# Kernel tuning notes

Measured on AMD Instinct MI355X. Metric: run time of the kernel, lower is better.

The kernel has to match this reference:

```python
import jax, jax.numpy as jnp
import numpy as np

B, N, IN_DIM, HID = 8, 4096, 256, 256


def setup_inputs() -> dict:
    key = jax.random.key(0)
    ks = jax.random.split(key, 7)
    s_in = 1.0 / np.sqrt(IN_DIM)
    return {
        "x": jax.random.normal(ks[0], (B, N, IN_DIM), dtype=jnp.float32),
        "Wq": jax.random.uniform(ks[1], (IN_DIM, HID), jnp.float32, -s_in, s_in),
        "bq": jax.random.uniform(ks[2], (HID,), jnp.float32, -s_in, s_in),
        "Wk": jax.random.uniform(ks[3], (IN_DIM, HID), jnp.float32, -s_in, s_in),
        "bk": jax.random.uniform(ks[4], (HID,), jnp.float32, -s_in, s_in),
        "Wv": jax.random.uniform(ks[5], (IN_DIM, HID), jnp.float32, -s_in, s_in),
        "bv": jax.random.uniform(ks[6], (HID,), jnp.float32, -s_in, s_in),
    }


def reference(x, Wq, bq, Wk, bk, Wv, bv):
    # x: [B, N, in_dim]
    Q = jnp.einsum("bnd,dh->bnh", x, Wq) + bq  # [B, N, H]
    K = jnp.einsum("bnd,dh->bnh", x, Wk) + bk
    V = jnp.einsum("bnd,dh->bnh", x, Wv) + bv
    scale = 1.0 / jnp.sqrt(jnp.asarray(K.shape[-1], dtype=x.dtype))
    scores = jnp.einsum("bqh,bkh->bqk", Q, K) * scale  # [B, N, N]
    attn = jax.nn.softmax(scores, axis=-1)
    out = jnp.einsum("bqk,bkh->bqh", attn, V)  # [B, N, H]
    return out.mean(axis=1)  # [B, H]
```

## Files before the change

### kernel.cpp

```cpp
#include <hip/hip_runtime.h>
#include <hip/hip_bf16.h>


#define NTOK 4096
#define HDIM 256
#define NBATCH 8
#define SCALE 0.0625f

typedef __attribute__((ext_vector_type(8))) short short8_t;
typedef __attribute__((ext_vector_type(16))) float f32x16;

__device__ __forceinline__ unsigned short f2bf(float f) {
    unsigned u = __float_as_uint(f);
    u += 0x7fff + ((u >> 16) & 1);
    return (unsigned short)(u >> 16);
}

#define MFMA(a, b, c) __builtin_amdgcn_mfma_f32_32x32x16_bf16(a, b, c, 0, 0, 0)

__device__ __forceinline__ void async_cp16(const void* g, void* l) {
    __builtin_amdgcn_global_load_lds((const __attribute__((address_space(1))) void*)g,
                                     (__attribute__((address_space(3))) void*)l, 16, 0, 0);
}

__device__ __forceinline__ void stage_swz(unsigned short* lds, const unsigned short* src,
                                          int row0, int dbase, int w, int l) {
#pragma unroll
    for (int i = 0; i < 4; ++i) {
        int rloc = w * 32 + i * 8 + (l >> 3);
        int u = (l & 7) ^ (l >> 3);
        const unsigned short* g = src + (size_t)(row0 + rloc) * HDIM + dbase + u * 8;
        unsigned short* d = lds + (w * 32 + i * 8) * 64;
        async_cp16(g, d);
    }
}

__device__ __forceinline__ short8_t frd(const unsigned short* lds, int rb, int lo, int u) {
    return *(const short8_t*)(lds + ((rb * 32 + lo) * 8 + (u ^ (lo & 7))) * 8);
}

__global__ void zero_kernel(float* __restrict__ w, float* __restrict__ l, float* __restrict__ out) {
    int i = blockIdx.x * 256 + threadIdx.x;
    w[i] = 0.f;
    l[i] = 0.f;
    if (i < NBATCH * HDIM) out[i] = 0.f;
}

__global__ void convert_x(const float* __restrict__ x, unsigned short* __restrict__ xbf) {
    int i = (blockIdx.x * 256 + threadIdx.x) * 4;
    float4 v = *(const float4*)(x + i);
    ushort4 o;
    o.x = f2bf(v.x); o.y = f2bf(v.y); o.z = f2bf(v.z); o.w = f2bf(v.w);
    *(ushort4*)(xbf + i) = o;
}

__global__ void convert_wt(const float* __restrict__ Wq, const float* __restrict__ Wk,
                           const float* __restrict__ Wv, unsigned short* __restrict__ Wt) {
    int z = blockIdx.y;
    const float* W = (z == 0) ? Wq : (z == 1) ? Wk : Wv;
    unsigned short* o = Wt + z * 65536;
    int n = threadIdx.x;
    for (int kk = 0; kk < 32; ++kk) {
        int k = blockIdx.x * 32 + kk;
        o[n * 256 + k] = f2bf(W[k * 256 + n]);
    }
}

__global__ __launch_bounds__(256) void qkv_mfma(const unsigned short* __restrict__ xbf,
                                                const unsigned short* __restrict__ Wt,
                                                const float* __restrict__ bq, const float* __restrict__ bk,
                                                const float* __restrict__ bv,
                                                unsigned short* __restrict__ Qbf,
                                                unsigned short* __restrict__ Kbf,
                                                float* __restrict__ Vf) {
    const int z = blockIdx.z;
    const unsigned short* Wz = Wt + z * 65536;
    const float* bias = (z == 0) ? bq : (z == 1) ? bk : bv;
    const int m0 = blockIdx.x * 128, n0 = blockIdx.y * 128;
    const int t = threadIdx.x, w = t >> 6, l = t & 63, lo = l & 31, hi = l >> 5;
    const int rm = (w & 1) * 2, rn = (w >> 1) * 2;

    __shared__ __align__(16) char smem[32768];
    unsigned short* Xb = (unsigned short*)smem;
    unsigned short* Wb = (unsigned short*)(smem + 16384);

    f32x16 acc[2][2];
#pragma unroll
    for (int a = 0; a < 2; ++a)
#pragma unroll
        for (int c = 0; c < 2; ++c)
#pragma unroll
            for (int r = 0; r < 16; ++r) acc[a][c][r] = 0.f;

    for (int dc = 0; dc < 4; ++dc) {
        __syncthreads();
        stage_swz(Xb, xbf, m0, dc * 64, w, l);
        stage_swz(Wb, Wz, n0, dc * 64, w, l);
        __syncthreads();
#pragma unroll
        for (int ks = 0; ks < 4; ++ks) {
            int u = ks * 2 + hi;
            short8_t a0 = frd(Xb, rm + 0, lo, u);
            short8_t a1 = frd(Xb, rm + 1, lo, u);
            short8_t b0 = frd(Wb, rn + 0, lo, u);
            short8_t b1 = frd(Wb, rn + 1, lo, u);
            acc[0][0] = MFMA(a0, b0, acc[0][0]);
            acc[0][1] = MFMA(a0, b1, acc[0][1]);
            acc[1][0] = MFMA(a1, b0, acc[1][0]);
            acc[1][1] = MFMA(a1, b1, acc[1][1]);
        }
    }
    float bc0 = bias[n0 + (w >> 1) * 64 + lo];
    float bc1 = bias[n0 + (w >> 1) * 64 + 32 + lo];
#pragma unroll
    for (int mb = 0; mb < 2; ++mb)
#pragma unroll
        for (int r = 0; r < 16; ++r) {
            int row = m0 + (w & 1) * 64 + mb * 32 + (r & 3) + 8 * (r >> 2) + 4 * hi;
            int c0 = n0 + (w >> 1) * 64 + lo, c1 = c0 + 32;
            float v0 = acc[mb][0][r] + bc0;
            float v1 = acc[mb][1][r] + bc1;
            if (z == 2) {
                Vf[(size_t)row * HDIM + c0] = v0;
                Vf[(size_t)row * HDIM + c1] = v1;
            } else {
                unsigned short* o = (z == 0) ? Qbf : Kbf;
                o[(size_t)row * HDIM + c0] = f2bf(v0);
                o[(size_t)row * HDIM + c1] = f2bf(v1);
            }
        }
}

__global__ __launch_bounds__(256) void score_pass1(const unsigned short* __restrict__ Qbf,
                                                   const unsigned short* __restrict__ Kbf,
                                                   float* __restrict__ lsum) {
    const int b = blockIdx.z;
    const int q0 = blockIdx.x * 128;
    const int kslice = blockIdx.y;
    const int t = threadIdx.x, w = t >> 6, l = t & 63, lo = l & 31, hi = l >> 5;
    const int rq = (w & 1) * 2, rk = (w >> 1) * 2;
    const unsigned short* Qb = Qbf + (size_t)b * NTOK * HDIM;
    const unsigned short* Kb = Kbf + (size_t)b * NTOK * HDIM;

    __shared__ __align__(16) char smem[33792];
    unsigned short* Qs = (unsigned short*)smem;
    unsigned short* Ks = Qs + 8192;
    float* red = (float*)smem;

    float rs[2][16];
#pragma unroll
    for (int mb = 0; mb < 2; ++mb)
#pragma unroll
        for (int r = 0; r < 16; ++r) rs[mb][r] = 0.f;

    for (int kt = 0; kt < 4; ++kt) {
        const int k0 = kslice * 512 + kt * 128;
        f32x16 acc[2][2];
#pragma unroll
        for (int a = 0; a < 2; ++a)
#pragma unroll
            for (int c = 0; c < 2; ++c)
#pragma unroll
                for (int r = 0; r < 16; ++r) acc[a][c][r] = 0.f;

        for (int dc = 0; dc < 4; ++dc) {
            __syncthreads();
            stage_swz(Qs, Qb, q0, dc * 64, w, l);
            stage_swz(Ks, Kb, k0, dc * 64, w, l);
            __syncthreads();
#pragma unroll
            for (int ks = 0; ks < 4; ++ks) {
                int u = ks * 2 + hi;
                short8_t a0 = frd(Qs, rq + 0, lo, u);
                short8_t a1 = frd(Qs, rq + 1, lo, u);
                short8_t b0 = frd(Ks, rk + 0, lo, u);
                short8_t b1 = frd(Ks, rk + 1, lo, u);
                acc[0][0] = MFMA(a0, b0, acc[0][0]);
                acc[0][1] = MFMA(a0, b1, acc[0][1]);
                acc[1][0] = MFMA(a1, b0, acc[1][0]);
                acc[1][1] = MFMA(a1, b1, acc[1][1]);
            }
        }
#pragma unroll
        for (int mb = 0; mb < 2; ++mb)
#pragma unroll
            for (int r = 0; r < 16; ++r)
                rs[mb][r] += __expf(acc[mb][0][r] * SCALE) + __expf(acc[mb][1][r] * SCALE);
    }
    __syncthreads();
#pragma unroll
    for (int mb = 0; mb < 2; ++mb)
#pragma unroll
        for (int r = 0; r < 16; ++r) {
            int row = (w & 1) * 64 + mb * 32 + (r & 3) + 8 * (r >> 2) + 4 * hi;
            red[row * 66 + (w >> 1) * 32 + lo] = rs[mb][r];
        }
    __syncthreads();
    if (t < 128) {
        float s = 0.f;
#pragma unroll 8
        for (int j = 0; j < 64; ++j) s += red[t * 66 + j];
        atomicAdd(&lsum[b * NTOK + q0 + t], s);
    }
}

__global__ __launch_bounds__(256) void score_pass2(const unsigned short* __restrict__ Qbf,
                                                   const unsigned short* __restrict__ Kbf,
                                                   const float* __restrict__ lsum,
                                                   float* __restrict__ wsum) {
    const int b = blockIdx.z;
    const int k0 = blockIdx.x * 128;
    const int qslice = blockIdx.y;
    const int t = threadIdx.x, w = t >> 6, l = t & 63, lo = l & 31, hi = l >> 5;
    const int rq = (w & 1) * 2, rk = (w >> 1) * 2;
    const unsigned short* Qb = Qbf + (size_t)b * NTOK * HDIM;
    const unsigned short* Kb = Kbf + (size_t)b * NTOK * HDIM;

    __shared__ __align__(16) char smem[33792];
    __shared__ float linv_s[128];
    unsigned short* Qs = (unsigned short*)smem;
    unsigned short* Ks = Qs + 8192;
    float* red2 = (float*)smem;

    float cs0 = 0.f, cs1 = 0.f;

    for (int qt = 0; qt < 4; ++qt) {
        const int q0 = qslice * 512 + qt * 128;
        f32x16 acc[2][2];
#pragma unroll
        for (int a = 0; a < 2; ++a)
#pragma unroll
            for (int c = 0; c < 2; ++c)
#pragma unroll
                for (int r = 0; r < 16; ++r) acc[a][c][r] = 0.f;

        for (int dc = 0; dc < 4; ++dc) {
            __syncthreads();
            stage_swz(Qs, Qb, q0, dc * 64, w, l);
            stage_swz(Ks, Kb, k0, dc * 64, w, l);
            if (dc == 0 && t < 128) linv_s[t] = 1.0f / lsum[b * NTOK + q0 + t];
            __syncthreads();
#pragma unroll
            for (int ks = 0; ks < 4; ++ks) {
                int u = ks * 2 + hi;
                short8_t a0 = frd(Qs, rq + 0, lo, u);
                short8_t a1 = frd(Qs, rq + 1, lo, u);
                short8_t b0 = frd(Ks, rk + 0, lo, u);
                short8_t b1 = frd(Ks, rk + 1, lo, u);
                acc[0][0] = MFMA(a0, b0, acc[0][0]);
                acc[0][1] = MFMA(a0, b1, acc[0][1]);
                acc[1][0] = MFMA(a1, b0, acc[1][0]);
                acc[1][1] = MFMA(a1, b1, acc[1][1]);
            }
        }
#pragma unroll
        for (int mb = 0; mb < 2; ++mb)
#pragma unroll
            for (int r = 0; r < 16; ++r) {
                float li = linv_s[(w & 1) * 64 + mb * 32 + (r & 3) + 8 * (r >> 2) + 4 * hi];
                cs0 += __expf(acc[mb][0][r] * SCALE) * li;
                cs1 += __expf(acc[mb][1][r] * SCALE) * li;
            }
    }
    __syncthreads();
    red2[((w >> 1) * 64 + lo) * 5 + (w & 1) * 2 + hi] = cs0;
    red2[((w >> 1) * 64 + 32 + lo) * 5 + (w & 1) * 2 + hi] = cs1;
    __syncthreads();
    if (t < 128) {
        float s = red2[t * 5 + 0] + red2[t * 5 + 1] + red2[t * 5 + 2] + red2[t * 5 + 3];
        atomicAdd(&wsum[b * NTOK + k0 + t], s);
    }
}

__global__ __launch_bounds__(256) void finalize_kernel(const float* __restrict__ V,
                                                       const float* __restrict__ w,
                                                       float* __restrict__ out) {
    const int b = blockIdx.y;
    const int k0 = blockIdx.x * 256;
    const int h = threadIdx.x;
    __shared__ float wsh[256];
    wsh[h] = w[b * NTOK + k0 + h];
    __syncthreads();
    const float* Vb = V + ((size_t)b * NTOK + k0) * HDIM;
    float acc = 0.f;
#pragma unroll 4
    for (int kk = 0; kk < 256; ++kk) acc = fmaf(wsh[kk], Vb[(size_t)kk * HDIM + h], acc);
    atomicAdd(&out[b * HDIM + h], acc * (1.0f / (float)NTOK));
}

extern "C" void kernel_launch(void* const* d_in, const int* in_sizes, int n_in,
                              void* d_out, int out_size, void* d_ws, size_t ws_size,
                              hipStream_t stream) {
    const float* x  = (const float*)d_in[0];
    const float* Wq = (const float*)d_in[1];
    const float* bq = (const float*)d_in[2];
    const float* Wk = (const float*)d_in[3];
    const float* bk = (const float*)d_in[4];
    const float* Wv = (const float*)d_in[5];
    const float* bv = (const float*)d_in[6];
    float* out = (float*)d_out;

    const size_t BNH = (size_t)NBATCH * NTOK * HDIM;
    unsigned short* Wt  = (unsigned short*)d_ws;
    unsigned short* xbf = Wt + 3 * 65536;
    unsigned short* Qbf = xbf + BNH;
    unsigned short* Kbf = Qbf + BNH;
    float* Vf   = (float*)(Kbf + BNH);
    float* lsum = Vf + BNH;
    float* wsum = lsum + (size_t)NBATCH * NTOK;

    zero_kernel<<<dim3(128), dim3(256), 0, stream>>>(wsum, lsum, out);
    convert_x<<<dim3(8192), dim3(256), 0, stream>>>(x, xbf);
    convert_wt<<<dim3(8, 3), dim3(256), 0, stream>>>(Wq, Wk, Wv, Wt);
    qkv_mfma<<<dim3(256, 2, 3), dim3(256), 0, stream>>>(xbf, Wt, bq, bk, bv, Qbf, Kbf, Vf);
    score_pass1<<<dim3(32, 8, 8), dim3(256), 0, stream>>>(Qbf, Kbf, lsum);
    score_pass2<<<dim3(32, 8, 8), dim3(256), 0, stream>>>(Qbf, Kbf, lsum, wsum);
    finalize_kernel<<<dim3(16, 8), dim3(256), 0, stream>>>(Vf, wsum, out);
}
```

Measured before the change: 294.6 us.

## Double-buffer Q/K LDS tiles in score passes to overlap loads with MFMA

Both score passes now ping-pong between two LDS buffers for the Q and K chunks. The next chunk is prefetched asynchronously while MFMAs run on the current one, and the two __syncthreads per chunk become a single waitcnt+barrier. The intent is to hide global-to-LDS load latency behind compute. The cost is doubling LDS to 64KB per block, which can lower occupancy, and a full vmcnt(0) wait each step that may limit how much overlap is achieved.

```diff
diff --git a/kernel.cpp b/kernel.cpp
--- a/kernel.cpp
+++ b/kernel.cpp
@@ -17,6 +17,11 @@
 }
 
 #define MFMA(a, b, c) __builtin_amdgcn_mfma_f32_32x32x16_bf16(a, b, c, 0, 0, 0)
+
+#define PIPE_BARRIER() do { \
+    asm volatile("s_waitcnt vmcnt(0) lgkmcnt(0)" ::: "memory"); \
+    asm volatile("s_barrier" ::: "memory"); \
+} while (0)
 
 __device__ __forceinline__ void async_cp16(const void* g, void* l) {
     __builtin_amdgcn_global_load_lds((const __attribute__((address_space(1))) void*)g,
@@ -136,15 +141,13 @@
                                                    float* __restrict__ lsum) {
     const int b = blockIdx.z;
     const int q0 = blockIdx.x * 128;
-    const int kslice = blockIdx.y;
+    const int kbase = blockIdx.y * 512;
     const int t = threadIdx.x, w = t >> 6, l = t & 63, lo = l & 31, hi = l >> 5;
     const int rq = (w & 1) * 2, rk = (w >> 1) * 2;
     const unsigned short* Qb = Qbf + (size_t)b * NTOK * HDIM;
     const unsigned short* Kb = Kbf + (size_t)b * NTOK * HDIM;
 
-    __shared__ __align__(16) char smem[33792];
-    unsigned short* Qs = (unsigned short*)smem;
-    unsigned short* Ks = Qs + 8192;
+    __shared__ __align__(16) char smem[65536];
     float* red = (float*)smem;
 
     float rs[2][16];
@@ -153,21 +156,32 @@
 #pragma unroll
         for (int r = 0; r < 16; ++r) rs[mb][r] = 0.f;
 
+    f32x16 acc[2][2];
+
+    stage_swz((unsigned short*)smem, Qb, q0, 0, w, l);
+    stage_swz((unsigned short*)(smem + 32768), Kb, kbase, 0, w, l);
+
     for (int kt = 0; kt < 4; ++kt) {
-        const int k0 = kslice * 512 + kt * 128;
-        f32x16 acc[2][2];
-#pragma unroll
-        for (int a = 0; a < 2; ++a)
-#pragma unroll
-            for (int c = 0; c < 2; ++c)
-#pragma unroll
-                for (int r = 0; r < 16; ++r) acc[a][c][r] = 0.f;
-
+#pragma unroll
         for (int dc = 0; dc < 4; ++dc) {
-            __syncthreads();
-            stage_swz(Qs, Qb, q0, dc * 64, w, l);
-            stage_swz(Ks, Kb, k0, dc * 64, w, l);
-            __syncthreads();
+            PIPE_BARRIER();
+            if (dc == 0) {
+#pragma unroll
+                for (int a = 0; a < 2; ++a)
+#pragma unroll
+                    for (int c = 0; c < 2; ++c)
+#pragma unroll
+                        for (int r = 0; r < 16; ++r) acc[a][c][r] = 0.f;
+            }
+            if (kt * 4 + dc < 15) {
+                const int ndc = (dc + 1) & 3;
+                const int nkt = kt + (dc == 3);
+                stage_swz((unsigned short*)(smem + (ndc & 1) * 16384), Qb, q0, ndc * 64, w, l);
+                stage_swz((unsigned short*)(smem + 32768 + (ndc & 1) * 16384), Kb,
+                          kbase + nkt * 128, ndc * 64, w, l);
+            }
+            const unsigned short* Qs = (const unsigned short*)(smem + (dc & 1) * 16384);
+            const unsigned short* Ks = (const unsigned short*)(smem + 32768 + (dc & 1) * 16384);
 #pragma unroll
             for (int ks = 0; ks < 4; ++ks) {
                 int u = ks * 2 + hi;
@@ -180,12 +194,14 @@
                 acc[1][0] = MFMA(a1, b0, acc[1][0]);
                 acc[1][1] = MFMA(a1, b1, acc[1][1]);
             }
-        }
-#pragma unroll
-        for (int mb = 0; mb < 2; ++mb)
-#pragma unroll
-            for (int r = 0; r < 16; ++r)
-                rs[mb][r] += __expf(acc[mb][0][r] * SCALE) + __expf(acc[mb][1][r] * SCALE);
+            if (dc == 3) {
+#pragma unroll
+                for (int mb = 0; mb < 2; ++mb)
+#pragma unroll
+                    for (int r = 0; r < 16; ++r)
+                        rs[mb][r] += __expf(acc[mb][0][r] * SCALE) + __expf(acc[mb][1][r] * SCALE);
+            }
+        }
     }
     __syncthreads();
 #pragma unroll
@@ -210,36 +226,47 @@
                                                    float* __restrict__ wsum) {
     const int b = blockIdx.z;
     const int k0 = blockIdx.x * 128;
-    const int qslice = blockIdx.y;
+    const int qbase = blockIdx.y * 512;
     const int t = threadIdx.x, w = t >> 6, l = t & 63, lo = l & 31, hi = l >> 5;
     const int rq = (w & 1) * 2, rk = (w >> 1) * 2;
     const unsigned short* Qb = Qbf + (size_t)b * NTOK * HDIM;
     const unsigned short* Kb = Kbf + (size_t)b * NTOK * HDIM;
 
-    __shared__ __align__(16) char smem[33792];
-    __shared__ float linv_s[128];
-    unsigned short* Qs = (unsigned short*)smem;
-    unsigned short* Ks = Qs + 8192;
+    __shared__ __align__(16) char smem[65536];
+    __shared__ float linv_s[2][128];
     float* red2 = (float*)smem;
 
     float cs0 = 0.f, cs1 = 0.f;
-
-    for (int qt = 0; qt < 4; ++qt) {
-        const int q0 = qslice * 512 + qt * 128;
-        f32x16 acc[2][2];
-#pragma unroll
-        for (int a = 0; a < 2; ++a)
-#pragma unroll
-            for (int c = 0; c < 2; ++c)
-#pragma unroll
-                for (int r = 0; r < 16; ++r) acc[a][c][r] = 0.f;
-
+    f32x16 acc[2][2];
+
+    stage_swz((unsigned short*)smem, Qb, qbase, 0, w, l);
+    stage_swz((unsigned short*)(smem + 32768), Kb, k0, 0, w, l);
+    if (t < 128) linv_s[0][t] = 1.0f / lsum[b * NTOK + qbase + t];
+
+    for (int kt = 0; kt < 4; ++kt) {
+#pragma unroll
         for (int dc = 0; dc < 4; ++dc) {
-            __syncthreads();
-            stage_swz(Qs, Qb, q0, dc * 64, w, l);
-            stage_swz(Ks, Kb, k0, dc * 64, w, l);
-            if (dc == 0 && t < 128) linv_s[t] = 1.0f / lsum[b * NTOK + q0 + t];
-            __syncthreads();
+            PIPE_BARRIER();
+            if (dc == 0) {
+#pragma unroll
+                for (int a = 0; a < 2; ++a)
+#pragma unroll
+                    for (int c = 0; c < 2; ++c)
+#pragma unroll
+                        for (int r = 0; r < 16; ++r) acc[a][c][r] = 0.f;
+            }
+            if (kt * 4 + dc < 15) {
+                const int ndc = (dc + 1) & 3;
+                const int nkt = kt + (dc == 3);
+                stage_swz((unsigned short*)(smem + (ndc & 1) * 16384), Qb,
+                          qbase + nkt * 128, ndc * 64, w, l);
+                stage_swz((unsigned short*)(smem + 32768 + (ndc & 1) * 16384), Kb,
+                          k0, ndc * 64, w, l);
+                if (ndc == 0 && t < 128)
+                    linv_s[nkt & 1][t] = 1.0f / lsum[b * NTOK + qbase + nkt * 128 + t];
+            }
+            const unsigned short* Qs = (const unsigned short*)(smem + (dc & 1) * 16384);
+            const unsigned short* Ks = (const unsigned short*)(smem + 32768 + (dc & 1) * 16384);
 #pragma unroll
             for (int ks = 0; ks < 4; ++ks) {
                 int u = ks * 2 + hi;
@@ -252,15 +279,17 @@
                 acc[1][0] = MFMA(a1, b0, acc[1][0]);
                 acc[1][1] = MFMA(a1, b1, acc[1][1]);
             }
-        }
-#pragma unroll
-        for (int mb = 0; mb < 2; ++mb)
-#pragma unroll
-            for (int r = 0; r < 16; ++r) {
-                float li = linv_s[(w & 1) * 64 + mb * 32 + (r & 3) + 8 * (r >> 2) + 4 * hi];
-                cs0 += __expf(acc[mb][0][r] * SCALE) * li;
-                cs1 += __expf(acc[mb][1][r] * SCALE) * li;
-            }
+            if (dc == 3) {
+#pragma unroll
+                for (int mb = 0; mb < 2; ++mb)
+#pragma unroll
+                    for (int r = 0; r < 16; ++r) {
+                        float li = linv_s[kt & 1][(w & 1) * 64 + mb * 32 + (r & 3) + 8 * (r >> 2) + 4 * hi];
+                        cs0 += __expf(acc[mb][0][r] * SCALE) * li;
+                        cs1 += __expf(acc[mb][1][r] * SCALE) * li;
+                    }
+            }
+        }
     }
     __syncthreads();
     red2[((w >> 1) * 64 + lo) * 5 + (w & 1) * 2 + hi] = cs0;
```

Result: slower. 303.0 us (+2.8%).
